# Kernel tuning notes

Measured on AMD Instinct MI355X. Metric: run time of the kernel, lower is better.

The kernel has to match this reference:

```python
import jax, jax.numpy as jnp
import numpy as np
import math

N = 100000   # outputSize (memory bank rows)
D = 128      # inputSize (feature dim)
B = 128      # batch size
K = 4096     # number of negatives per sample
T = 0.07     # temperature
MOMENTUM = 0.5


def setup_inputs() -> dict:
    key = jax.random.key(0)
    k1, k2, k3, k4, k5 = jax.random.split(key, 5)
    stdv = 1.0 / math.sqrt(D / 3.0)
    # l2-normalized features, as produced by the encoder in contrastive setups
    v1 = jax.random.normal(k1, (B, D), dtype=jnp.float32)
    v1 = v1 / jnp.linalg.norm(v1, axis=1, keepdims=True)
    v2 = jax.random.normal(k2, (B, D), dtype=jnp.float32)
    v2 = v2 / jnp.linalg.norm(v2, axis=1, keepdims=True)
    idx = jax.random.randint(k3, (B, K + 1), 0, N, dtype=jnp.int32)  # pos+neg bank rows
    y = jnp.arange(B, dtype=jnp.int32)  # distinct positive slots (first-visit behavior)
    # memory buffers initialized U(-stdv, stdv), as in torch.rand*2*stdv - stdv
    memory_v1 = jax.random.uniform(k4, (N, D), dtype=jnp.float32, minval=-stdv, maxval=stdv)
    memory_v2 = jax.random.uniform(k5, (N, D), dtype=jnp.float32, minval=-stdv, maxval=stdv)
    return {"v1": v1, "v2": v2, "idx": idx, "y": y,
            "memory_v1": memory_v1, "memory_v2": memory_v2}


def reference(v1, v2, idx, y, memory_v1, memory_v2):
    n_out = memory_v1.shape[0]
    # gather K+1 rows per sample (detached in the original -> stop_gradient)
    w1 = jax.lax.stop_gradient(memory_v1[idx])  # [B, K+1, D]
    w2 = jax.lax.stop_gradient(memory_v2[idx])  # [B, K+1, D]
    # batched vector-matrix product + exp/T
    out_v2 = jnp.exp(jnp.einsum('bkd,bd->bk', w1, v2) / T)  # [B, K+1]
    out_v1 = jnp.exp(jnp.einsum('bkd,bd->bk', w2, v1) / T)  # [B, K+1]
    # normalization constants (first-call Z computation: mean * outputSize)
    Z_v1 = jax.lax.stop_gradient(out_v1.mean()) * n_out
    Z_v2 = jax.lax.stop_gradient(out_v2.mean()) * n_out
    out_v1 = out_v1 / Z_v1
    out_v2 = out_v2 / Z_v2
    # momentum-blended normalize-and-scatter memory update (no_grad in torch)
    upd1 = MOMENTUM * memory_v1[y] + (1.0 - MOMENTUM) * v1  # [B, D]
    upd1 = upd1 / jnp.linalg.norm(upd1, axis=1, keepdims=True)
    new_memory_v1 = memory_v1.at[y].set(upd1)
    upd2 = MOMENTUM * memory_v2[y] + (1.0 - MOMENTUM) * v2
    upd2 = upd2 / jnp.linalg.norm(upd2, axis=1, keepdims=True)
    new_memory_v2 = memory_v2.at[y].set(upd2)
    return out_v1, out_v2, new_memory_v1, new_memory_v2
```

## Files before the change

kernel.cpp:

```cpp
#include <hip/hip_runtime.h>
#include <math.h>

constexpr int N_ROWS = 100000;
constexpr int D      = 128;
constexpr int B      = 128;
constexpr int KP1    = 4097;
constexpr int TOTAL_PAIRS = B * KP1;
constexpr float INV_T = 1.0f / 0.07f;

__global__ void init_ws_kernel(float* ws) {
    if (threadIdx.x < 2) ws[threadIdx.x] = 0.0f;
}

__global__ __launch_bounds__(256) void score_kernel(
    const float* __restrict__ v1, const float* __restrict__ v2,
    const int* __restrict__ idx,
    const float* __restrict__ mem1, const float* __restrict__ mem2,
    float* __restrict__ out,
    float* __restrict__ sums)
{
    const int l   = threadIdx.x & 31;
    const int grp = threadIdx.x >> 5;
    const int n_groups = gridDim.x * 8;
    int g = blockIdx.x * 8 + grp;

    const float4* __restrict__ m1 = (const float4*)mem1;
    const float4* __restrict__ m2 = (const float4*)mem2;
    const float4* __restrict__ a1p = (const float4*)v1;
    const float4* __restrict__ a2p = (const float4*)v2;

    float acc1 = 0.0f, acc2 = 0.0f;

    for (int p = g; p < TOTAL_PAIRS; p += n_groups) {
        int row = idx[p];
        unsigned b = (unsigned)p / (unsigned)KP1;

        float4 w1 = m1[(size_t)row * 32 + l];
        float4 w2 = m2[(size_t)row * 32 + l];
        float4 a1 = a1p[b * 32 + l];
        float4 a2 = a2p[b * 32 + l];

        float d1 = w2.x * a1.x + w2.y * a1.y + w2.z * a1.z + w2.w * a1.w;
        float d2 = w1.x * a2.x + w1.y * a2.y + w1.z * a2.z + w1.w * a2.w;

        #pragma unroll
        for (int off = 16; off >= 1; off >>= 1) {
            d1 += __shfl_xor(d1, off);
            d2 += __shfl_xor(d2, off);
        }

        if (l == 0) {
            float e1 = __expf(d1 * INV_T);
            float e2 = __expf(d2 * INV_T);
            out[p]               = e1;
            out[TOTAL_PAIRS + p] = e2;
            acc1 += e1;
            acc2 += e2;
        }
    }

    __shared__ float s1[8], s2[8];
    if (l == 0) { s1[grp] = acc1; s2[grp] = acc2; }
    __syncthreads();
    if (threadIdx.x == 0) {
        float t1 = 0.0f, t2 = 0.0f;
        #pragma unroll
        for (int i = 0; i < 8; ++i) { t1 += s1[i]; t2 += s2[i]; }
        atomicAdd(&sums[0], t1);
        atomicAdd(&sums[1], t2);
    }
}

__global__ __launch_bounds__(256) void scale_kernel(
    float* __restrict__ out, const float* __restrict__ sums)
{
    int i = blockIdx.x * blockDim.x + threadIdx.x;
    if (i >= 2 * TOTAL_PAIRS) return;
    float s = (i < TOTAL_PAIRS) ? sums[0] : sums[1];
    float sc = (float)((double)TOTAL_PAIRS / ((double)s * (double)N_ROWS));
    out[i] *= sc;
}

__global__ __launch_bounds__(256) void copy_mem_kernel(
    const float4* __restrict__ m1, const float4* __restrict__ m2,
    float4* __restrict__ o1, float4* __restrict__ o2)
{
    const int n4 = N_ROWS * (D / 4);
    for (int i = blockIdx.x * blockDim.x + threadIdx.x; i < n4;
         i += gridDim.x * blockDim.x) {
        o1[i] = m1[i];
        o2[i] = m2[i];
    }
}

__global__ __launch_bounds__(64) void update_rows_kernel(
    const float* __restrict__ v1, const float* __restrict__ v2,
    const int* __restrict__ y,
    const float* __restrict__ mem1, const float* __restrict__ mem2,
    float* __restrict__ o1, float* __restrict__ o2)
{
    int b    = blockIdx.x & (B - 1);
    int bank = blockIdx.x >> 7;
    int lane = threadIdx.x;

    const float2* __restrict__ m = (const float2*)(bank ? mem2 : mem1);
    const float2* __restrict__ v = (const float2*)(bank ? v2 : v1);
    float2* __restrict__ o       = (float2*)(bank ? o2 : o1);

    int row = y[b];
    float2 mv = m[(size_t)row * 64 + lane];
    float2 vv = v[b * 64 + lane];
    float2 u;
    u.x = 0.5f * mv.x + 0.5f * vv.x;
    u.y = 0.5f * mv.y + 0.5f * vv.y;

    float ss = u.x * u.x + u.y * u.y;
    #pragma unroll
    for (int off = 32; off >= 1; off >>= 1)
        ss += __shfl_xor(ss, off);

    float inv = 1.0f / sqrtf(ss);
    float2 r; r.x = u.x * inv; r.y = u.y * inv;
    o[(size_t)row * 64 + lane] = r;
}

extern "C" void kernel_launch(void* const* d_in, const int* in_sizes, int n_in,
                              void* d_out, int out_size, void* d_ws, size_t ws_size,
                              hipStream_t stream) {
    const float* v1   = (const float*)d_in[0];
    const float* v2   = (const float*)d_in[1];
    const int*   idx  = (const int*)d_in[2];
    const int*   y    = (const int*)d_in[3];
    const float* mem1 = (const float*)d_in[4];
    const float* mem2 = (const float*)d_in[5];

    float* out = (float*)d_out;
    float* out_mem1 = out + 2 * (size_t)TOTAL_PAIRS;
    float* out_mem2 = out_mem1 + (size_t)N_ROWS * D;
    float* sums = (float*)d_ws;

    init_ws_kernel<<<1, 64, 0, stream>>>(sums);

    score_kernel<<<1024, 256, 0, stream>>>(v1, v2, idx, mem1, mem2, out, sums);

    scale_kernel<<<(2 * TOTAL_PAIRS + 255) / 256, 256, 0, stream>>>(out, sums);

    copy_mem_kernel<<<2048, 256, 0, stream>>>(
        (const float4*)mem1, (const float4*)mem2,
        (float4*)out_mem1, (float4*)out_mem2);

    update_rows_kernel<<<2 * B, 64, 0, stream>>>(
        v1, v2, y, mem1, mem2, out_mem1, out_mem2);
}
```

Baseline: 297.0 us.

## Fuse score and memory copy into one kernel, merge scale with row update

Odd blocks copy the memory banks while even blocks compute the scores, so the gather-bound scoring and the bandwidth-bound copy run concurrently in one launch. Each wave group is pinned to a single batch row, which lets the query vectors stay in registers, and the loop is unrolled by two to keep more gathers in flight. The scale pass and the momentum row update are merged into one grid-stride kernel, cutting launches from five to three. The copy and score blocks now compete for memory bandwidth, and the update blocks in the finish kernel rely on the copy having completed in the earlier launch.

```diff
diff --git a/kernel.cpp b/kernel.cpp
--- a/kernel.cpp
+++ b/kernel.cpp
@@ -7,55 +7,101 @@
 constexpr int KP1    = 4097;
 constexpr int TOTAL_PAIRS = B * KP1;
 constexpr float INV_T = 1.0f / 0.07f;
+constexpr int N4 = N_ROWS * (D / 4);
+
+constexpr int SC_BLOCKS = 1024;
+constexpr int CP_BLOCKS = 1024;
 
 __global__ void init_ws_kernel(float* ws) {
     if (threadIdx.x < 2) ws[threadIdx.x] = 0.0f;
 }
 
-__global__ __launch_bounds__(256) void score_kernel(
+__device__ __forceinline__ float dot4(float4 a, float4 b) {
+    return a.x * b.x + a.y * b.y + a.z * b.z + a.w * b.w;
+}
+
+__device__ __forceinline__ float red32(float v) {
+    #pragma unroll
+    for (int off = 16; off >= 1; off >>= 1) v += __shfl_xor(v, off);
+    return v;
+}
+
+__global__ __launch_bounds__(256) void mega_kernel(
     const float* __restrict__ v1, const float* __restrict__ v2,
     const int* __restrict__ idx,
     const float* __restrict__ mem1, const float* __restrict__ mem2,
     float* __restrict__ out,
-    float* __restrict__ sums)
+    float* __restrict__ sums,
+    float4* __restrict__ o1, float4* __restrict__ o2)
 {
+    if (blockIdx.x & 1) {
+        int cid = blockIdx.x >> 1;
+        const float4* __restrict__ m1 = (const float4*)mem1;
+        const float4* __restrict__ m2 = (const float4*)mem2;
+        int tid = cid * 256 + threadIdx.x;
+        int stride = CP_BLOCKS * 256;
+        for (int i = tid; i < N4; i += stride) {
+            o1[i] = m1[i];
+            o2[i] = m2[i];
+        }
+        return;
+    }
+
+    const int sid = blockIdx.x >> 1;
     const int l   = threadIdx.x & 31;
     const int grp = threadIdx.x >> 5;
-    const int n_groups = gridDim.x * 8;
-    int g = blockIdx.x * 8 + grp;
+    const int g   = sid * 8 + grp;
+    const int b   = g >> 6;
+    const int gk  = g & 63;
 
     const float4* __restrict__ m1 = (const float4*)mem1;
     const float4* __restrict__ m2 = (const float4*)mem2;
-    const float4* __restrict__ a1p = (const float4*)v1;
-    const float4* __restrict__ a2p = (const float4*)v2;
+    const float4 a1 = ((const float4*)v1)[b * 32 + l];
+    const float4 a2 = ((const float4*)v2)[b * 32 + l];
+    const int base = b * KP1;
 
     float acc1 = 0.0f, acc2 = 0.0f;
+    int k = gk;
+    for (; k + 64 < KP1; k += 128) {
+        int p0 = base + k, p1 = base + k + 64;
+        int r0 = idx[p0], r1 = idx[p1];
+        float4 w10 = m1[(size_t)r0 * 32 + l];
+        float4 w20 = m2[(size_t)r0 * 32 + l];
+        float4 w11 = m1[(size_t)r1 * 32 + l];
+        float4 w21 = m2[(size_t)r1 * 32 + l];
 
-    for (int p = g; p < TOTAL_PAIRS; p += n_groups) {
-        int row = idx[p];
-        unsigned b = (unsigned)p / (unsigned)KP1;
-
-        float4 w1 = m1[(size_t)row * 32 + l];
-        float4 w2 = m2[(size_t)row * 32 + l];
-        float4 a1 = a1p[b * 32 + l];
-        float4 a2 = a2p[b * 32 + l];
-
-        float d1 = w2.x * a1.x + w2.y * a1.y + w2.z * a1.z + w2.w * a1.w;
-        float d2 = w1.x * a2.x + w1.y * a2.y + w1.z * a2.z + w1.w * a2.w;
-
-        #pragma unroll
-        for (int off = 16; off >= 1; off >>= 1) {
-            d1 += __shfl_xor(d1, off);
-            d2 += __shfl_xor(d2, off);
-        }
+        float d10 = red32(dot4(w20, a1));
+        float d20 = red32(dot4(w10, a2));
+        float d11 = red32(dot4(w21, a1));
+        float d21 = red32(dot4(w11, a2));
 
         if (l == 0) {
-            float e1 = __expf(d1 * INV_T);
-            float e2 = __expf(d2 * INV_T);
-            out[p]               = e1;
-            out[TOTAL_PAIRS + p] = e2;
-            acc1 += e1;
-            acc2 += e2;
+            float e10 = __expf(d10 * INV_T);
+            float e20 = __expf(d20 * INV_T);
+            float e11 = __expf(d11 * INV_T);
+            float e21 = __expf(d21 * INV_T);
+            out[p0]               = e10;
+            out[TOTAL_PAIRS + p0] = e20;
+            out[p1]               = e11;
+            out[TOTAL_PAIRS + p1] = e21;
+            acc1 += e10 + e11;
+            acc2 += e20 + e21;
+        }
+    }
+    for (; k < KP1; k += 64) {
+        int p0 = base + k;
+        int r0 = idx[p0];
+        float4 w10 = m1[(size_t)r0 * 32 + l];
+        float4 w20 = m2[(size_t)r0 * 32 + l];
+        float d10 = red32(dot4(w20, a1));
+        float d20 = red32(dot4(w10, a2));
+        if (l == 0) {
+            float e10 = __expf(d10 * INV_T);
+            float e20 = __expf(d20 * INV_T);
+            out[p0]               = e10;
+            out[TOTAL_PAIRS + p0] = e20;
+            acc1 += e10;
+            acc2 += e20;
         }
     }
 
@@ -71,57 +117,41 @@
     }
 }
 
-__global__ __launch_bounds__(256) void scale_kernel(
-    float* __restrict__ out, const float* __restrict__ sums)
-{
-    int i = blockIdx.x * blockDim.x + threadIdx.x;
-    if (i >= 2 * TOTAL_PAIRS) return;
-    float s = (i < TOTAL_PAIRS) ? sums[0] : sums[1];
-    float sc = (float)((double)TOTAL_PAIRS / ((double)s * (double)N_ROWS));
-    out[i] *= sc;
-}
-
-__global__ __launch_bounds__(256) void copy_mem_kernel(
-    const float4* __restrict__ m1, const float4* __restrict__ m2,
-    float4* __restrict__ o1, float4* __restrict__ o2)
-{
-    const int n4 = N_ROWS * (D / 4);
-    for (int i = blockIdx.x * blockDim.x + threadIdx.x; i < n4;
-         i += gridDim.x * blockDim.x) {
-        o1[i] = m1[i];
-        o2[i] = m2[i];
-    }
-}
-
-__global__ __launch_bounds__(64) void update_rows_kernel(
+__global__ __launch_bounds__(256) void finish_kernel(
+    float* __restrict__ out, const float* __restrict__ sums,
     const float* __restrict__ v1, const float* __restrict__ v2,
     const int* __restrict__ y,
     const float* __restrict__ mem1, const float* __restrict__ mem2,
     float* __restrict__ o1, float* __restrict__ o2)
 {
-    int b    = blockIdx.x & (B - 1);
-    int bank = blockIdx.x >> 7;
-    int lane = threadIdx.x;
+    if (blockIdx.x < 2 * B && threadIdx.x < 64) {
+        int b    = blockIdx.x & (B - 1);
+        int bank = blockIdx.x >> 7;
+        int lane = threadIdx.x;
+        const float2* __restrict__ m = (const float2*)(bank ? mem2 : mem1);
+        const float2* __restrict__ v = (const float2*)(bank ? v2 : v1);
+        float2* __restrict__ o       = (float2*)(bank ? o2 : o1);
+        int row = y[b];
+        float2 mv = m[(size_t)row * 64 + lane];
+        float2 vv = v[b * 64 + lane];
+        float2 u;
+        u.x = 0.5f * mv.x + 0.5f * vv.x;
+        u.y = 0.5f * mv.y + 0.5f * vv.y;
+        float ss = u.x * u.x + u.y * u.y;
+        #pragma unroll
+        for (int off = 32; off >= 1; off >>= 1) ss += __shfl_xor(ss, off);
+        float inv = 1.0f / sqrtf(ss);
+        float2 r; r.x = u.x * inv; r.y = u.y * inv;
+        o[(size_t)row * 64 + lane] = r;
+    }
 
-    const float2* __restrict__ m = (const float2*)(bank ? mem2 : mem1);
-    const float2* __restrict__ v = (const float2*)(bank ? v2 : v1);
-    float2* __restrict__ o       = (float2*)(bank ? o2 : o1);
-
-    int row = y[b];
-    float2 mv = m[(size_t)row * 64 + lane];
-    float2 vv = v[b * 64 + lane];
-    float2 u;
-    u.x = 0.5f * mv.x + 0.5f * vv.x;
-    u.y = 0.5f * mv.y + 0.5f * vv.y;
-
-    float ss = u.x * u.x + u.y * u.y;
-    #pragma unroll
-    for (int off = 32; off >= 1; off >>= 1)
-        ss += __shfl_xor(ss, off);
-
-    float inv = 1.0f / sqrtf(ss);
-    float2 r; r.x = u.x * inv; r.y = u.y * inv;
-    o[(size_t)row * 64 + lane] = r;
+    float sc1 = (float)((double)TOTAL_PAIRS / ((double)sums[0] * (double)N_ROWS));
+    float sc2 = (float)((double)TOTAL_PAIRS / ((double)sums[1] * (double)N_ROWS));
+    int stride = gridDim.x * blockDim.x;
+    for (int i = blockIdx.x * blockDim.x + threadIdx.x; i < 2 * TOTAL_PAIRS;
+         i += stride) {
+        out[i] *= (i < TOTAL_PAIRS) ? sc1 : sc2;
+    }
 }
 
 extern "C" void kernel_launch(void* const* d_in, const int* in_sizes, int n_in,
@@ -141,14 +171,10 @@
 
     init_ws_kernel<<<1, 64, 0, stream>>>(sums);
 
-    score_kernel<<<1024, 256, 0, stream>>>(v1, v2, idx, mem1, mem2, out, sums);
-
-    scale_kernel<<<(2 * TOTAL_PAIRS + 255) / 256, 256, 0, stream>>>(out, sums);
-
-    copy_mem_kernel<<<2048, 256, 0, stream>>>(
-        (const float4*)mem1, (const float4*)mem2,
+    mega_kernel<<<SC_BLOCKS + CP_BLOCKS, 256, 0, stream>>>(
+        v1, v2, idx, mem1, mem2, out, sums,
         (float4*)out_mem1, (float4*)out_mem2);
 
-    update_rows_kernel<<<2 * B, 64, 0, stream>>>(
-        v1, v2, y, mem1, mem2, out_mem1, out_mem2);
+    finish_kernel<<<1024, 256, 0, stream>>>(
+        out, sums, v1, v2, y, mem1, mem2, out_mem1, out_mem2);
 }
```

After: 287.5 us. 1.03x faster.

## Precompute all bank-row scores with bf16 MFMA GEMM, then gather by index

Applied to the files above, without the earlier changes.

Instead of gathering 128*4097 rows of 128 floats per bank, the code runs a dense bf16 MFMA GEMM of both memory banks against all 128 query vectors. The resulting scores are packed as bf16 pairs into scratch space that aliases the output memory region. A gather kernel then looks up the score for each (idx, batch) pair, applies exp and accumulates the normalization sums. The copy of memory_v2 is fused into the GEMM kernel, and the copy of memory_v1 is fused with the scaling pass, which overwrites the scratch area afterwards. Scores now come from bf16 inputs and outputs, so precision drops, and exp(x/0.07) amplifies those errors.

```diff
diff --git a/kernel.cpp b/kernel.cpp
--- a/kernel.cpp
+++ b/kernel.cpp
@@ -7,90 +7,139 @@
 constexpr int KP1    = 4097;
 constexpr int TOTAL_PAIRS = B * KP1;
 constexpr float INV_T = 1.0f / 0.07f;
-
-__global__ void init_ws_kernel(float* ws) {
-    if (threadIdx.x < 2) ws[threadIdx.x] = 0.0f;
-}
-
-__global__ __launch_bounds__(256) void score_kernel(
+constexpr int N4 = N_ROWS * (D / 4);
+
+typedef __attribute__((ext_vector_type(8))) short short8;
+typedef __attribute__((ext_vector_type(4))) float f32x4;
+
+__device__ __forceinline__ unsigned short f2bf(float f) {
+    union { float f; unsigned u; } x; x.f = f;
+    unsigned r = x.u + 0x7fffu + ((x.u >> 16) & 1u);
+    return (unsigned short)(r >> 16);
+}
+__device__ __forceinline__ float bf2f(unsigned short h) {
+    union { unsigned u; float f; } x; x.u = ((unsigned)h) << 16;
+    return x.f;
+}
+__device__ __forceinline__ short8 cvt8(float4 a, float4 b) {
+    short8 r;
+    r[0] = (short)f2bf(a.x); r[1] = (short)f2bf(a.y);
+    r[2] = (short)f2bf(a.z); r[3] = (short)f2bf(a.w);
+    r[4] = (short)f2bf(b.x); r[5] = (short)f2bf(b.y);
+    r[6] = (short)f2bf(b.z); r[7] = (short)f2bf(b.w);
+    return r;
+}
+
+__global__ __launch_bounds__(256) void init_kernel(
     const float* __restrict__ v1, const float* __restrict__ v2,
-    const int* __restrict__ idx,
+    unsigned short* __restrict__ vbf,
+    float* __restrict__ sums)
+{
+    int tid = blockIdx.x * 256 + threadIdx.x;
+    vbf[tid]         = f2bf(v1[tid]);
+    vbf[16384 + tid] = f2bf(v2[tid]);
+    if (tid < 2) sums[tid] = 0.0f;
+}
+
+__global__ __launch_bounds__(256) void gemm_kernel(
     const float* __restrict__ mem1, const float* __restrict__ mem2,
-    float* __restrict__ out,
-    float* __restrict__ sums)
-{
-    const int l   = threadIdx.x & 31;
-    const int grp = threadIdx.x >> 5;
-    const int n_groups = gridDim.x * 8;
-    int g = blockIdx.x * 8 + grp;
-
-    const float4* __restrict__ m1 = (const float4*)mem1;
-    const float4* __restrict__ m2 = (const float4*)mem2;
-    const float4* __restrict__ a1p = (const float4*)v1;
-    const float4* __restrict__ a2p = (const float4*)v2;
-
-    float acc1 = 0.0f, acc2 = 0.0f;
-
-    for (int p = g; p < TOTAL_PAIRS; p += n_groups) {
+    const unsigned short* __restrict__ vbf,
+    unsigned* __restrict__ SS,
+    const float4* __restrict__ m2_4, float4* __restrict__ o2_4)
+{
+    const int wg   = blockIdx.x;
+    const int wave = threadIdx.x >> 6;
+    const int lane = threadIdx.x & 63;
+    const int quad = lane >> 4;
+    const int lr   = lane & 15;
+    const int m0   = wg * 64 + wave * 16;
+
+    int am = m0 + lr; if (am > N_ROWS - 1) am = N_ROWS - 1;
+    const float4* r1 = (const float4*)(mem1 + (size_t)am * 128);
+    const float4* r2 = (const float4*)(mem2 + (size_t)am * 128);
+    short8 a1[4], a2[4];
+    #pragma unroll
+    for (int s = 0; s < 4; ++s) {
+        int c4 = s * 8 + quad * 2;
+        a1[s] = cvt8(r1[c4], r1[c4 + 1]);
+        a2[s] = cvt8(r2[c4], r2[c4 + 1]);
+    }
+
+    const short8* vb = (const short8*)vbf;
+
+    #pragma unroll
+    for (int ct = 0; ct < 8; ++ct) {
+        const int n0 = ct * 16;
+        f32x4 acc1 = {0.f, 0.f, 0.f, 0.f};
+        f32x4 acc2 = {0.f, 0.f, 0.f, 0.f};
+        #pragma unroll
+        for (int s = 0; s < 4; ++s) {
+            short8 b1 = vb[(n0 + lr) * 16 + s * 4 + quad];
+            short8 b2 = vb[2048 + (n0 + lr) * 16 + s * 4 + quad];
+            acc1 = __builtin_amdgcn_mfma_f32_16x16x32_bf16(a2[s], b1, acc1, 0, 0, 0);
+            acc2 = __builtin_amdgcn_mfma_f32_16x16x32_bf16(a1[s], b2, acc2, 0, 0, 0);
+        }
+        #pragma unroll
+        for (int r = 0; r < 4; ++r) {
+            int m = m0 + quad * 4 + r;
+            if (m < N_ROWS) {
+                unsigned pk = (unsigned)f2bf(acc1[r]) |
+                              ((unsigned)f2bf(acc2[r]) << 16);
+                SS[(size_t)m * 128 + n0 + lr] = pk;
+            }
+        }
+    }
+
+    const int base4 = wg * 2048;
+    #pragma unroll
+    for (int j = 0; j < 8; ++j) {
+        int i = base4 + j * 256 + threadIdx.x;
+        if (i < N4) o2_4[i] = m2_4[i];
+    }
+}
+
+__global__ __launch_bounds__(256) void gather_kernel(
+    const int* __restrict__ idx, const unsigned* __restrict__ SS,
+    float* __restrict__ out, float* __restrict__ sums)
+{
+    int p = blockIdx.x * 256 + threadIdx.x;
+    float e1 = 0.0f, e2 = 0.0f;
+    if (p < TOTAL_PAIRS) {
+        int b   = (int)((unsigned)p / (unsigned)KP1);
         int row = idx[p];
-        unsigned b = (unsigned)p / (unsigned)KP1;
-
-        float4 w1 = m1[(size_t)row * 32 + l];
-        float4 w2 = m2[(size_t)row * 32 + l];
-        float4 a1 = a1p[b * 32 + l];
-        float4 a2 = a2p[b * 32 + l];
-
-        float d1 = w2.x * a1.x + w2.y * a1.y + w2.z * a1.z + w2.w * a1.w;
-        float d2 = w1.x * a2.x + w1.y * a2.y + w1.z * a2.z + w1.w * a2.w;
-
-        #pragma unroll
-        for (int off = 16; off >= 1; off >>= 1) {
-            d1 += __shfl_xor(d1, off);
-            d2 += __shfl_xor(d2, off);
-        }
-
-        if (l == 0) {
-            float e1 = __expf(d1 * INV_T);
-            float e2 = __expf(d2 * INV_T);
-            out[p]               = e1;
-            out[TOTAL_PAIRS + p] = e2;
-            acc1 += e1;
-            acc2 += e2;
-        }
-    }
-
-    __shared__ float s1[8], s2[8];
-    if (l == 0) { s1[grp] = acc1; s2[grp] = acc2; }
+        unsigned pk = SS[(size_t)row * 128 + b];
+        e1 = __expf(bf2f((unsigned short)(pk & 0xffffu)) * INV_T);
+        e2 = __expf(bf2f((unsigned short)(pk >> 16)) * INV_T);
+        out[p]               = e1;
+        out[TOTAL_PAIRS + p] = e2;
+    }
+    #pragma unroll
+    for (int off = 32; off >= 1; off >>= 1) {
+        e1 += __shfl_xor(e1, off);
+        e2 += __shfl_xor(e2, off);
+    }
+    __shared__ float s1[4], s2[4];
+    const int wave = threadIdx.x >> 6;
+    if ((threadIdx.x & 63) == 0) { s1[wave] = e1; s2[wave] = e2; }
     __syncthreads();
     if (threadIdx.x == 0) {
-        float t1 = 0.0f, t2 = 0.0f;
-        #pragma unroll
-        for (int i = 0; i < 8; ++i) { t1 += s1[i]; t2 += s2[i]; }
-        atomicAdd(&sums[0], t1);
-        atomicAdd(&sums[1], t2);
-    }
-}
-
-__global__ __launch_bounds__(256) void scale_kernel(
+        atomicAdd(&sums[0], s1[0] + s1[1] + s1[2] + s1[3]);
+        atomicAdd(&sums[1], s2[0] + s2[1] + s2[2] + s2[3]);
+    }
+}
+
+__global__ __launch_bounds__(256) void copy_scale_kernel(
+    const float4* __restrict__ m1_4, float4* __restrict__ o1_4,
     float* __restrict__ out, const float* __restrict__ sums)
 {
-    int i = blockIdx.x * blockDim.x + threadIdx.x;
-    if (i >= 2 * TOTAL_PAIRS) return;
-    float s = (i < TOTAL_PAIRS) ? sums[0] : sums[1];
-    float sc = (float)((double)TOTAL_PAIRS / ((double)s * (double)N_ROWS));
-    out[i] *= sc;
-}
-
-__global__ __launch_bounds__(256) void copy_mem_kernel(
-    const float4* __restrict__ m1, const float4* __restrict__ m2,
-    float4* __restrict__ o1, float4* __restrict__ o2)
-{
-    const int n4 = N_ROWS * (D / 4);
-    for (int i = blockIdx.x * blockDim.x + threadIdx.x; i < n4;
-         i += gridDim.x * blockDim.x) {
-        o1[i] = m1[i];
-        o2[i] = m2[i];
-    }
+    const int stride = gridDim.x * 256;
+    const int t = blockIdx.x * 256 + threadIdx.x;
+    for (int i = t; i < N4; i += stride) o1_4[i] = m1_4[i];
+
+    float sc1 = (float)((double)TOTAL_PAIRS / ((double)sums[0] * (double)N_ROWS));
+    float sc2 = (float)((double)TOTAL_PAIRS / ((double)sums[1] * (double)N_ROWS));
+    for (int i = t; i < 2 * TOTAL_PAIRS; i += stride)
+        out[i] *= (i < TOTAL_PAIRS) ? sc1 : sc2;
 }
 
 __global__ __launch_bounds__(64) void update_rows_kernel(
@@ -102,23 +151,18 @@
     int b    = blockIdx.x & (B - 1);
     int bank = blockIdx.x >> 7;
     int lane = threadIdx.x;
-
     const float2* __restrict__ m = (const float2*)(bank ? mem2 : mem1);
     const float2* __restrict__ v = (const float2*)(bank ? v2 : v1);
     float2* __restrict__ o       = (float2*)(bank ? o2 : o1);
-
     int row = y[b];
     float2 mv = m[(size_t)row * 64 + lane];
     float2 vv = v[b * 64 + lane];
     float2 u;
     u.x = 0.5f * mv.x + 0.5f * vv.x;
     u.y = 0.5f * mv.y + 0.5f * vv.y;
-
     float ss = u.x * u.x + u.y * u.y;
     #pragma unroll
-    for (int off = 32; off >= 1; off >>= 1)
-        ss += __shfl_xor(ss, off);
-
+    for (int off = 32; off >= 1; off >>= 1) ss += __shfl_xor(ss, off);
     float inv = 1.0f / sqrtf(ss);
     float2 r; r.x = u.x * inv; r.y = u.y * inv;
     o[(size_t)row * 64 + lane] = r;
@@ -134,20 +178,24 @@
     const float* mem1 = (const float*)d_in[4];
     const float* mem2 = (const float*)d_in[5];
 
-    float* out = (float*)d_out;
+    float* out      = (float*)d_out;
     float* out_mem1 = out + 2 * (size_t)TOTAL_PAIRS;
     float* out_mem2 = out_mem1 + (size_t)N_ROWS * D;
-    float* sums = (float*)d_ws;
-
-    init_ws_kernel<<<1, 64, 0, stream>>>(sums);
-
-    score_kernel<<<1024, 256, 0, stream>>>(v1, v2, idx, mem1, mem2, out, sums);
-
-    scale_kernel<<<(2 * TOTAL_PAIRS + 255) / 256, 256, 0, stream>>>(out, sums);
-
-    copy_mem_kernel<<<2048, 256, 0, stream>>>(
-        (const float4*)mem1, (const float4*)mem2,
-        (float4*)out_mem1, (float4*)out_mem2);
+    float* sums     = (float*)d_ws;
+
+    unsigned short* vbf = (unsigned short*)d_out;
+    unsigned*       SS  = (unsigned*)out_mem1;
+
+    init_kernel<<<64, 256, 0, stream>>>(v1, v2, vbf, sums);
+
+    gemm_kernel<<<(N_ROWS + 63) / 64, 256, 0, stream>>>(
+        mem1, mem2, vbf, SS, (const float4*)mem2, (float4*)out_mem2);
+
+    gather_kernel<<<(TOTAL_PAIRS + 255) / 256, 256, 0, stream>>>(
+        idx, SS, out, sums);
+
+    copy_scale_kernel<<<2048, 256, 0, stream>>>(
+        (const float4*)mem1, (float4*)out_mem1, out, sums);
 
     update_rows_kernel<<<2 * B, 64, 0, stream>>>(
         v1, v2, y, mem1, mem2, out_mem1, out_mem2);
```

Result: slower. 318.3 us (+7.2%).
